# Kernel tuning notes

Hardware: AMD Instinct MI355X
Metric: run time of the kernel (lower is better)

The kernel has to match this reference:

```python
import jax, jax.numpy as jnp
import numpy as np

B, N, P_FEATS = 8, 4096, 3
WIDTH, HEADS, LAYERS, N_LAT = 768, 12, 8, 256
NUM_FREQS = 8
D_HEAD = WIDTH // HEADS
SCALE = 1.0 / np.sqrt(np.sqrt(D_HEAD))  # applied to q and k separately
IN_DIM = 3 * (1 + 2 * NUM_FREQS) + P_FEATS  # 54
EPS = 1e-5


def fourier_embed(pc):
    # pc: [B,N,3] -> [B,N,51] (include_input + sin/cos at freqs 2^0..2^7)
    freqs = (2.0 ** jnp.arange(NUM_FREQS)).astype(pc.dtype)
    ang = pc[..., None] * freqs  # [B,N,3,F]
    ang = ang.reshape(*pc.shape[:-1], 3 * NUM_FREQS)
    return jnp.concatenate([pc, jnp.sin(ang), jnp.cos(ang)], axis=-1)


def layernorm(x, s, b):
    mu = jnp.mean(x, axis=-1, keepdims=True)
    var = jnp.mean(jnp.square(x - mu), axis=-1, keepdims=True)
    return (x - mu) * jax.lax.rsqrt(var + EPS) * s + b


def mh_attn(q, k, v):
    # q: [B,T,H,C], k/v: [B,S,H,C]
    w = jnp.einsum('bthc,bshc->bhts', q * SCALE, k * SCALE)
    w = jax.nn.softmax(w.astype(jnp.float32), axis=-1).astype(q.dtype)
    out = jnp.einsum('bhts,bshc->bthc', w, v)
    return out.reshape(*q.shape[:2], -1)


def setup_inputs() -> dict:
    key = jax.random.key(0)
    ks = iter(jax.random.split(key, 64))
    rn = lambda shape, std=0.02: jax.random.normal(next(ks), shape, jnp.float32) * std
    inp = {
        'pc': jax.random.normal(next(ks), (B, N, 3), jnp.float32),
        'feats': jax.random.uniform(next(ks), (B, N, P_FEATS), jnp.float32),
        'query': rn((N_LAT, WIDTH)),
        'in_W': rn((WIDTH, IN_DIM)), 'in_b': jnp.zeros((WIDTH,)),
        'ca_qkv_W': rn((3 * WIDTH, WIDTH)), 'ca_qkv_b': jnp.zeros((3 * WIDTH,)),
        'ca_proj_W': rn((WIDTH, WIDTH)), 'ca_proj_b': jnp.zeros((WIDTH,)),
        'ln1_s': jnp.ones((LAYERS, WIDTH)), 'ln1_b': jnp.zeros((LAYERS, WIDTH)),
        'qkv_W': rn((LAYERS, 3 * WIDTH, WIDTH)), 'qkv_b': jnp.zeros((LAYERS, 3 * WIDTH)),
        'proj_W': rn((LAYERS, WIDTH, WIDTH)), 'proj_b': jnp.zeros((LAYERS, WIDTH)),
        'ln2_s': jnp.ones((LAYERS, WIDTH)), 'ln2_b': jnp.zeros((LAYERS, WIDTH)),
        'fc_W': rn((LAYERS, 4 * WIDTH, WIDTH)), 'fc_b': jnp.zeros((LAYERS, 4 * WIDTH)),
        'fc2_W': rn((LAYERS, WIDTH, 4 * WIDTH)), 'fc2_b': jnp.zeros((LAYERS, WIDTH)),
    }
    return inp


def _forward(pc, feats, query, in_W, in_b, ca_qkv_W, ca_qkv_b, ca_proj_W, ca_proj_b,
             ln1_s, ln1_b, qkv_W, qkv_b, proj_W, proj_b, ln2_s, ln2_b,
             fc_W, fc_b, fc2_W, fc2_b):
    bs = pc.shape[0]
    data = jnp.concatenate([fourier_embed(pc), feats], axis=-1)  # [B,N,54]
    data = data @ in_W.T + in_b  # [B,N,W]
    q_lat = jnp.broadcast_to(query[None], (bs, N_LAT, WIDTH))

    # --- cross attention (no residual, matching source) ---
    q = (q_lat @ ca_qkv_W.T + ca_qkv_b)[..., :WIDTH]
    kv = data @ ca_qkv_W.T + ca_qkv_b
    k, v = kv[..., WIDTH:2 * WIDTH], kv[..., 2 * WIDTH:]
    q = q.reshape(bs, N_LAT, HEADS, D_HEAD)
    k = k.reshape(bs, N, HEADS, D_HEAD)
    v = v.reshape(bs, N, HEADS, D_HEAD)
    latents = mh_attn(q, k, v) @ ca_proj_W.T + ca_proj_b  # [B,L,W]

    # --- self-attention transformer stack via scan ---
    def block(x, p):
        (l1s, l1b, qW, qb, pW, pb, l2s, l2b, fW, fb, f2W, f2b) = p
        h = layernorm(x, l1s, l1b)
        qkv = (h @ qW.T + qb).reshape(bs, N_LAT, HEADS, 3 * D_HEAD)
        qh, kh, vh = jnp.split(qkv, 3, axis=-1)
        x = x + mh_attn(qh, kh, vh) @ pW.T + pb
        h = layernorm(x, l2s, l2b)
        h = jax.nn.gelu(h @ fW.T + fb, approximate=False) @ f2W.T + f2b
        return x + h, None

    params = (ln1_s, ln1_b, qkv_W, qkv_b, proj_W, proj_b, ln2_s, ln2_b, fc_W, fc_b, fc2_W, fc2_b)
    latents, _ = jax.lax.scan(block, latents, params)
    return latents, pc


def reference(pc, feats, query, in_W, in_b, ca_qkv_W, ca_qkv_b, ca_proj_W, ca_proj_b,
              ln1_s, ln1_b, qkv_W, qkv_b, proj_W, proj_b, ln2_s, ln2_b,
              fc_W, fc_b, fc2_W, fc2_b):
    return _forward(pc, feats, query, in_W, in_b, ca_qkv_W, ca_qkv_b, ca_proj_W, ca_proj_b,
                    ln1_s, ln1_b, qkv_W, qkv_b, proj_W, proj_b, ln2_s, ln2_b,
                    fc_W, fc_b, fc2_W, fc2_b)
```

## Files before the change

### kernel.cpp

```cpp
#include <hip/hip_runtime.h>
#include <stdint.h>

typedef unsigned short u16;
typedef __bf16 bf16x8 __attribute__((ext_vector_type(8)));
typedef float f32x4 __attribute__((ext_vector_type(4)));

#define DEVINL __device__ __forceinline__

DEVINL u16 f2bf(float f) {
  union { float f; unsigned u; } c; c.f = f;
  unsigned u = c.u + 0x7FFFu + ((c.u >> 16) & 1u);
  return (u16)(u >> 16);
}

DEVINL float bf2f(u16 v) {
  union { unsigned u; float f; } c; c.u = (unsigned)v << 16;
  return c.f;
}

DEVINL void gl2lds16(const void* g, void* l) {
  __builtin_amdgcn_global_load_lds(
      (const __attribute__((address_space(1))) unsigned int*)g,
      (__attribute__((address_space(3))) unsigned int*)l, 16, 0, 0);
}

__global__ __launch_bounds__(256) void cvt4_kernel(
    const float* __restrict__ s0, u16* __restrict__ d0, int n0,
    const float* __restrict__ s1, u16* __restrict__ d1, int n1,
    const float* __restrict__ s2, u16* __restrict__ d2, int n2,
    const float* __restrict__ s3, u16* __restrict__ d3, int n3) {
  int i = blockIdx.x * 256 + threadIdx.x;
  const float* s; u16* d;
  if (i < n0) { s = s0; d = d0; }
  else {
    i -= n0;
    if (i < n1) { s = s1; d = d1; }
    else {
      i -= n1;
      if (i < n2) { s = s2; d = d2; }
      else {
        i -= n2;
        if (i >= n3) return;
        s = s3; d = d3;
      }
    }
  }
  float4 v = ((const float4*)s)[i];
  unsigned a = (unsigned)f2bf(v.x) | ((unsigned)f2bf(v.y) << 16);
  unsigned b = (unsigned)f2bf(v.z) | ((unsigned)f2bf(v.w) << 16);
  ((uint2*)d)[i] = make_uint2(a, b);
}

__global__ __launch_bounds__(256) void pad_inw_kernel(const float* __restrict__ src,
                                                      u16* __restrict__ dst) {
  int t = blockIdx.x * 256 + threadIdx.x;
  int r = t >> 6, c = t & 63;
  dst[t] = (c < 54) ? f2bf(src[r * 54 + c]) : (u16)0;
}

__global__ __launch_bounds__(256) void embed_kernel(const float* __restrict__ pc,
                                                    const float* __restrict__ feats,
                                                    u16* __restrict__ emb) {
  int t = blockIdx.x * 256 + threadIdx.x;
  int p = t >> 6, c = t & 63;
  float v = 0.f;
  if (c < 3) {
    v = pc[p * 3 + c];
  } else if (c < 27) {
    int i = c - 3;
    float f = (float)(1 << (i & 7));
    v = sinf(pc[p * 3 + (i >> 3)] * f);
  } else if (c < 51) {
    int i = c - 27;
    float f = (float)(1 << (i & 7));
    v = cosf(pc[p * 3 + (i >> 3)] * f);
  } else if (c < 54) {
    v = feats[p * 3 + (c - 51)];
  }
  emb[t] = f2bf(v);
}

template <int TM, int TN, int WR, int WC, int MODE>
__global__ __launch_bounds__(256) void gemm_t(
    const u16* __restrict__ A, const u16* __restrict__ Bw,
    const float* __restrict__ bias, const float* __restrict__ resid,
    float* __restrict__ outF, u16* __restrict__ outB,
    int M, int N, int Nout, int K, int gelu,
    u16* __restrict__ vt, int vy, int skvt, int bsh) {
  constexpr int IM = TM / WR / 16;
  constexpr int IN = TN / WC / 16;
  __shared__ u16 As[TM * 32];
  __shared__ u16 Bs[TN * 32];
  const int tid = threadIdx.x;
  const int lane = tid & 63, w = tid >> 6;
  const int l15 = lane & 15, quad = lane >> 4;
  const int mblk = blockIdx.x * TM, nblk = blockIdx.y * TN;
  const int wm = (w % WR) * (TM / WR);
  const int wn = (w / WR) * (TN / WC);

  f32x4 acc[IM][IN];
#pragma unroll
  for (int i = 0; i < IM; i++)
#pragma unroll
    for (int j = 0; j < IN; j++) acc[i][j] = f32x4{0.f, 0.f, 0.f, 0.f};

  const bool tv = (MODE == 1) && ((int)blockIdx.y >= vy);

  if (!tv) {
    for (int k0 = 0; k0 < K; k0 += 32) {
#pragma unroll
      for (int s = tid; s < TM * 4; s += 256) {
        int row = s >> 2, c8 = (s & 3) << 3;
        gl2lds16(A + (size_t)(mblk + row) * K + (k0 + c8), &As[s * 8]);
      }
#pragma unroll
      for (int s = tid; s < TN * 4; s += 256) {
        int row = s >> 2, c8 = (s & 3) << 3;
        gl2lds16(Bw + (size_t)(nblk + row) * K + (k0 + c8), &Bs[s * 8]);
      }
      __syncthreads();
      bf16x8 af[IM], bfr[IN];
#pragma unroll
      for (int i = 0; i < IM; i++)
        af[i] = *(const bf16x8*)&As[(wm + i * 16 + l15) * 32 + quad * 8];
#pragma unroll
      for (int j = 0; j < IN; j++)
        bfr[j] = *(const bf16x8*)&Bs[(wn + j * 16 + l15) * 32 + quad * 8];
#pragma unroll
      for (int i = 0; i < IM; i++)
#pragma unroll
        for (int j = 0; j < IN; j++)
          acc[i][j] = __builtin_amdgcn_mfma_f32_16x16x32_bf16(bfr[j], af[i], acc[i][j], 0, 0, 0);
      __syncthreads();
    }
#pragma unroll
    for (int i = 0; i < IM; i++) {
      int m = mblk + wm + i * 16 + l15;
#pragma unroll
      for (int j = 0; j < IN; j++) {
        int n0 = nblk + wn + j * 16 + quad * 4;
        float4 bv = *(const float4*)&bias[n0];
        float v0 = acc[i][j][0] + bv.x;
        float v1 = acc[i][j][1] + bv.y;
        float v2 = acc[i][j][2] + bv.z;
        float v3 = acc[i][j][3] + bv.w;
        if (gelu) {
          v0 = 0.5f * v0 * (1.0f + erff(v0 * 0.70710678118f));
          v1 = 0.5f * v1 * (1.0f + erff(v1 * 0.70710678118f));
          v2 = 0.5f * v2 * (1.0f + erff(v2 * 0.70710678118f));
          v3 = 0.5f * v3 * (1.0f + erff(v3 * 0.70710678118f));
        }
        size_t idx = (size_t)m * Nout + n0;
        if (resid) {
          float4 rv = *(const float4*)&resid[idx];
          v0 += rv.x; v1 += rv.y; v2 += rv.z; v3 += rv.w;
        }
        if (outF) {
          float4 ov = {v0, v1, v2, v3};
          *(float4*)&outF[idx] = ov;
        }
        if (outB) {
          unsigned lo = (unsigned)f2bf(v0) | ((unsigned)f2bf(v1) << 16);
          unsigned hi = (unsigned)f2bf(v2) | ((unsigned)f2bf(v3) << 16);
          *(uint2*)&outB[idx] = make_uint2(lo, hi);
        }
      }
    }
  } else {
    for (int k0 = 0; k0 < K; k0 += 32) {
#pragma unroll
      for (int s = tid; s < TM * 4; s += 256) {
        int row = s >> 2, c8 = (s & 3) << 3;
        gl2lds16(A + (size_t)(mblk + row) * K + (k0 + c8), &As[s * 8]);
      }
#pragma unroll
      for (int s = tid; s < TN * 4; s += 256) {
        int row = s >> 2, c8 = (s & 3) << 3;
        gl2lds16(Bw + (size_t)(nblk + row) * K + (k0 + c8), &Bs[s * 8]);
      }
      __syncthreads();
      bf16x8 af[IM], bfr[IN];
#pragma unroll
      for (int i = 0; i < IM; i++)
        af[i] = *(const bf16x8*)&As[(wm + i * 16 + l15) * 32 + quad * 8];
#pragma unroll
      for (int j = 0; j < IN; j++)
        bfr[j] = *(const bf16x8*)&Bs[(wn + j * 16 + l15) * 32 + quad * 8];
#pragma unroll
      for (int i = 0; i < IM; i++)
#pragma unroll
        for (int j = 0; j < IN; j++)
          acc[i][j] = __builtin_amdgcn_mfma_f32_16x16x32_bf16(af[i], bfr[j], acc[i][j], 0, 0, 0);
      __syncthreads();
    }
    int msk = (1 << bsh) - 1;
#pragma unroll
    for (int j = 0; j < IN; j++) {
      int n = nblk + wn + j * 16 + l15;
      float bv = bias[n];
      int nv = n - vy * TN;
#pragma unroll
      for (int i = 0; i < IM; i++) {
        int m0 = mblk + wm + i * 16 + quad * 4;
        int b = m0 >> bsh;
        int s0 = m0 & msk;
        float v0 = acc[i][j][0] + bv;
        float v1 = acc[i][j][1] + bv;
        float v2 = acc[i][j][2] + bv;
        float v3 = acc[i][j][3] + bv;
        unsigned lo = (unsigned)f2bf(v0) | ((unsigned)f2bf(v1) << 16);
        unsigned hi = (unsigned)f2bf(v2) | ((unsigned)f2bf(v3) << 16);
        size_t addr = (size_t)(b * 768 + nv) * skvt + s0;
        *(uint2*)&vt[addr] = make_uint2(lo, hi);
      }
    }
  }
}

__global__ __launch_bounds__(256) void repack_vt_kernel(
    const u16* __restrict__ In, long bstride, int rs, int voff, int hs,
    u16* __restrict__ Vt, int Skv) {
  __shared__ u16 tile[64 * 65];
  int nst = Skv >> 6;
  int bid = blockIdx.x;
  int st = bid % nst;
  int bh = bid / nst;
  int h = bh % 12, b = bh / 12;
  const u16* src = In + (size_t)b * bstride + (size_t)(st * 64) * rs + voff + h * hs;
  int tid = threadIdx.x;
#pragma unroll
  for (int p = 0; p < 2; p++) {
    int slot = tid + p * 256;
    int s = slot >> 3, d8 = (slot & 7) << 3;
    uint4 v = *(const uint4*)(src + (size_t)s * rs + d8);
    u16 tmp[8];
    *(uint4*)tmp = v;
#pragma unroll
    for (int j = 0; j < 8; j++) tile[s * 65 + d8 + j] = tmp[j];
  }
  __syncthreads();
  u16* dst = Vt + ((size_t)(b * 12 + h) * 64) * Skv + st * 64;
#pragma unroll
  for (int p = 0; p < 2; p++) {
    int slot = tid + p * 256;
    int d = slot >> 3, s8 = (slot & 7) << 3;
    u16 tmp[8];
#pragma unroll
    for (int j = 0; j < 8; j++) tmp[j] = tile[(s8 + j) * 65 + d];
    *(uint4*)(dst + (size_t)d * Skv + s8) = *(uint4*)tmp;
  }
}

__global__ __launch_bounds__(256) void flash_kernel(
    const u16* __restrict__ Q, long qb, int qrs, int qhs,
    const u16* __restrict__ Kp, long kb, int krs, int khs,
    const u16* __restrict__ Vt, u16* __restrict__ Out,
    u16* __restrict__ Part, float* __restrict__ Ml,
    int Skv, int nsplit, int kvlen, float scale2) {
  __shared__ u16 Qs[64 * 64];
  __shared__ u16 Ks[64 * 64];
  __shared__ u16 Vs[64 * 64];
  __shared__ u16 Ps[64 * 72];

  const int tid = threadIdx.x;
  const int lane = tid & 63, w = tid >> 6;
  const int l15 = lane & 15, quad = lane >> 4;

  int bid = blockIdx.x;
  int per_bh = nsplit << 2;
  int bh = bid / per_bh;
  int rem = bid - bh * per_bh;
  int split = rem >> 2, qt = rem & 3;
  int h = bh % 12, b = bh / 12;

  const u16* Qbase = Q + (size_t)b * qb + (size_t)(qt * 64) * qrs + h * qhs;
  const u16* Kbase = Kp + (size_t)b * kb + (size_t)h * khs;
  const u16* Vbase = Vt + ((size_t)(b * 12 + h) * 64) * Skv;

#pragma unroll
  for (int p = 0; p < 2; ++p) {
    int slot = tid + p * 256;
    int row = slot >> 3, c = slot & 7;
    int cg = (c - row) & 7;
    gl2lds16(Qbase + (size_t)row * qrs + cg * 8, &Qs[slot * 8]);
  }
  __syncthreads();

  bf16x8 qa[2];
#pragma unroll
  for (int kk = 0; kk < 2; kk++)
    qa[kk] = *(const bf16x8*)&Qs[(w * 16 + l15) * 64 + ((kk * 4 + quad + l15) & 7) * 8];

  f32x4 zero = {0.f, 0.f, 0.f, 0.f};
  f32x4 O[4];
  float m_i[4], l_i[4];
#pragma unroll
  for (int d = 0; d < 4; d++) O[d] = zero;
#pragma unroll
  for (int r = 0; r < 4; r++) { m_i[r] = -1e30f; l_i[r] = 0.f; }

  int kt0 = split * kvlen;
  for (int kt = kt0; kt < kt0 + kvlen; kt += 64) {
#pragma unroll
    for (int p = 0; p < 2; ++p) {
      int slot = tid + p * 256;
      int row = slot >> 3, c = slot & 7;
      int cg = (c - row) & 7;
      gl2lds16(Kbase + (size_t)(kt + row) * krs + cg * 8, &Ks[slot * 8]);
      gl2lds16(Vbase + (size_t)row * Skv + kt + cg * 8, &Vs[slot * 8]);
    }
    __syncthreads();

    f32x4 S[4];
#pragma unroll
    for (int j = 0; j < 4; j++) S[j] = zero;
#pragma unroll
    for (int kk = 0; kk < 2; kk++) {
#pragma unroll
      for (int j = 0; j < 4; j++) {
        bf16x8 kf = *(const bf16x8*)&Ks[(j * 16 + l15) * 64 + ((kk * 4 + quad + l15) & 7) * 8];
        S[j] = __builtin_amdgcn_mfma_f32_16x16x32_bf16(qa[kk], kf, S[j], 0, 0, 0);
      }
    }
    float alpha[4];
#pragma unroll
    for (int r = 0; r < 4; r++) {
      float s0 = S[0][r] * scale2, s1 = S[1][r] * scale2;
      float s2 = S[2][r] * scale2, s3 = S[3][r] * scale2;
      S[0][r] = s0; S[1][r] = s1; S[2][r] = s2; S[3][r] = s3;
      float mx = fmaxf(fmaxf(s0, s1), fmaxf(s2, s3));
#pragma unroll
      for (int msk = 1; msk < 16; msk <<= 1) mx = fmaxf(mx, __shfl_xor(mx, msk, 64));
      float mnew = fmaxf(m_i[r], mx);
      float al = __expf(m_i[r] - mnew);
      m_i[r] = mnew;
      alpha[r] = al;
      float sum = 0.f;
#pragma unroll
      for (int j = 0; j < 4; j++) {
        float pv = __expf(S[j][r] - mnew);
        S[j][r] = pv;
        sum += pv;
      }
#pragma unroll
      for (int msk = 1; msk < 16; msk <<= 1) sum += __shfl_xor(sum, msk, 64);
      l_i[r] = l_i[r] * al + sum;
    }
#pragma unroll
    for (int j = 0; j < 4; j++)
#pragma unroll
      for (int r = 0; r < 4; r++)
        Ps[(w * 16 + quad * 4 + r) * 72 + j * 16 + l15] = f2bf(S[j][r]);
#pragma unroll
    for (int d = 0; d < 4; d++)
#pragma unroll
      for (int r = 0; r < 4; r++) O[d][r] *= alpha[r];
    __asm__ __volatile__("s_waitcnt lgkmcnt(0)" ::: "memory");
#pragma unroll
    for (int kk = 0; kk < 2; kk++) {
      bf16x8 pa = *(const bf16x8*)&Ps[(w * 16 + l15) * 72 + kk * 32 + quad * 8];
#pragma unroll
      for (int d = 0; d < 4; d++) {
        bf16x8 vf = *(const bf16x8*)&Vs[(d * 16 + l15) * 64 + ((kk * 4 + quad + l15) & 7) * 8];
        O[d] = __builtin_amdgcn_mfma_f32_16x16x32_bf16(pa, vf, O[d], 0, 0, 0);
      }
    }
    __syncthreads();
  }

  if (nsplit == 1) {
    u16* Ob = Out + ((size_t)(b * 256 + qt * 64 + w * 16 + quad * 4)) * 768 + h * 64 + l15;
#pragma unroll
    for (int d = 0; d < 4; d++)
#pragma unroll
      for (int r = 0; r < 4; r++) {
        float v = O[d][r] / l_i[r];
        Ob[(size_t)r * 768 + d * 16] = f2bf(v);
      }
  } else {
    u16* Pb = Part + ((size_t)(bh * 4 + qt) * nsplit + split) * 4096;
    int rowb = w * 16 + quad * 4;
#pragma unroll
    for (int d = 0; d < 4; d++)
#pragma unroll
      for (int r = 0; r < 4; r++)
        Pb[(rowb + r) * 64 + d * 16 + l15] = f2bf(O[d][r]);
    if (l15 == 0) {
      float* MlB = Ml + ((size_t)(bh * 4 + qt) * nsplit + split) * 128;
#pragma unroll
      for (int r = 0; r < 4; r++) {
        MlB[rowb + r] = m_i[r];
        MlB[64 + rowb + r] = l_i[r];
      }
    }
  }
}

__global__ __launch_bounds__(256) void freduce_kernel(
    const u16* __restrict__ Part, const float* __restrict__ Ml,
    u16* __restrict__ Out, int nsplit) {
  int bid = blockIdx.x;
  int qt = bid & 3, bh = bid >> 2;
  int h = bh % 12, b = bh / 12;
  int tid = threadIdx.x;
  int r = tid >> 2, dc = tid & 3;
  const float* mlb = Ml + (size_t)(bh * 4 + qt) * nsplit * 128;
  float M = -1e30f;
  for (int s = 0; s < nsplit; s++) M = fmaxf(M, mlb[s * 128 + r]);
  float L = 0.f;
  float accv[16];
#pragma unroll
  for (int i = 0; i < 16; i++) accv[i] = 0.f;
  const u16* pb = Part + (size_t)(bh * 4 + qt) * nsplit * 4096 + r * 64 + dc * 16;
  for (int s = 0; s < nsplit; s++) {
    float wgt = __expf(mlb[s * 128 + r] - M);
    L += wgt * mlb[s * 128 + 64 + r];
    u16 tmp[16];
    *(uint4*)tmp = *(const uint4*)(pb + s * 4096);
    *(uint4*)(tmp + 8) = *(const uint4*)(pb + s * 4096 + 8);
#pragma unroll
    for (int i = 0; i < 16; i++) accv[i] += wgt * bf2f(tmp[i]);
  }
  float inv = 1.f / L;
  u16 ot[16];
#pragma unroll
  for (int i = 0; i < 16; i++) ot[i] = f2bf(accv[i] * inv);
  u16* ob = Out + ((size_t)(b * 256 + qt * 64 + r)) * 768 + h * 64 + dc * 16;
  *(uint4*)ob = *(uint4*)ot;
  *(uint4*)(ob + 8) = *(uint4*)(ot + 8);
}

__global__ __launch_bounds__(256) void ln_kernel(const float* __restrict__ X,
                                                 const float* __restrict__ sc,
                                                 const float* __restrict__ bi,
                                                 u16* __restrict__ Hout) {
  int row = blockIdx.x;
  int tid = threadIdx.x;
  const float* x = X + (size_t)row * 768;
  float v0 = x[tid], v1 = x[tid + 256], v2 = x[tid + 512];
  float s = v0 + v1 + v2;
  float q = v0 * v0 + v1 * v1 + v2 * v2;
#pragma unroll
  for (int m = 1; m < 64; m <<= 1) {
    s += __shfl_xor(s, m, 64);
    q += __shfl_xor(q, m, 64);
  }
  __shared__ float rs[4], rq[4];
  if ((tid & 63) == 0) { rs[tid >> 6] = s; rq[tid >> 6] = q; }
  __syncthreads();
  s = rs[0] + rs[1] + rs[2] + rs[3];
  q = rq[0] + rq[1] + rq[2] + rq[3];
  float mu = s * (1.f / 768.f);
  float var = q * (1.f / 768.f) - mu * mu;
  float rstd = rsqrtf(var + 1e-5f);
  u16* ho = Hout + (size_t)row * 768;
  ho[tid]       = f2bf((v0 - mu) * rstd * sc[tid]       + bi[tid]);
  ho[tid + 256] = f2bf((v1 - mu) * rstd * sc[tid + 256] + bi[tid + 256]);
  ho[tid + 512] = f2bf((v2 - mu) * rstd * sc[tid + 512] + bi[tid + 512]);
}

__global__ __launch_bounds__(256) void copy4_kernel(const float* __restrict__ src,
                                                    float* __restrict__ dst, int n4) {
  int i = blockIdx.x * 256 + threadIdx.x;
  if (i < n4) ((float4*)dst)[i] = ((const float4*)src)[i];
}

extern "C" void kernel_launch(void* const* d_in, const int* in_sizes, int n_in,
                              void* d_out, int out_size, void* d_ws, size_t ws_size,
                              hipStream_t stream) {
  const float* pc        = (const float*)d_in[0];
  const float* feats     = (const float*)d_in[1];
  const float* query     = (const float*)d_in[2];
  const float* in_W      = (const float*)d_in[3];
  const float* in_b      = (const float*)d_in[4];
  const float* ca_qkv_W  = (const float*)d_in[5];
  const float* ca_qkv_b  = (const float*)d_in[6];
  const float* ca_proj_W = (const float*)d_in[7];
  const float* ca_proj_b = (const float*)d_in[8];
  const float* ln1_s     = (const float*)d_in[9];
  const float* ln1_b     = (const float*)d_in[10];
  const float* qkv_W     = (const float*)d_in[11];
  const float* qkv_b     = (const float*)d_in[12];
  const float* proj_W    = (const float*)d_in[13];
  const float* proj_b    = (const float*)d_in[14];
  const float* ln2_s     = (const float*)d_in[15];
  const float* ln2_b     = (const float*)d_in[16];
  const float* fc_W      = (const float*)d_in[17];
  const float* fc_b      = (const float*)d_in[18];
  const float* fc2_W     = (const float*)d_in[19];
  const float* fc2_b     = (const float*)d_in[20];

  char* base = (char*)d_ws;
  size_t off = 0;
  auto alloc = [&](size_t bytes) -> char* {
    char* p = base + off;
    off += (bytes + 255) & ~(size_t)255;
    return p;
  };

  u16* Wq      = (u16*)alloc(768 * 64 * 2);
  u16* Wquery  = (u16*)alloc(256 * 768 * 2);
  u16* Wcaqkv  = (u16*)alloc(2304 * 768 * 2);
  u16* Wcaproj = (u16*)alloc(768 * 768 * 2);
  u16* Wlqkv   = (u16*)alloc(2304 * 768 * 2);
  u16* Wlproj  = (u16*)alloc(768 * 768 * 2);
  u16* Wlfc    = (u16*)alloc(3072 * 768 * 2);
  u16* Wlfc2   = (u16*)alloc(768 * 3072 * 2);
  u16* qc      = (u16*)alloc(256 * 768 * 2);
  u16* attn    = (u16*)alloc((size_t)2048 * 768 * 2);
  u16* hbuf    = (u16*)alloc((size_t)2048 * 768 * 2);
  char* uni    = alloc(13369344);
  u16* qkvb    = (u16*)uni;
  u16* VtS     = (u16*)(uni + 9437184);
  u16* fc1     = (u16*)uni;
  u16* Part    = (u16*)uni;
  float* Ml    = (float*)(uni + 12582912);

  size_t fixed_end = off;
  size_t per_b = (size_t)4096 * 64 * 2 + 3 * ((size_t)4096 * 768 * 2);
  int CB;
  if (fixed_end + 8 * per_b + 4096 <= ws_size) CB = 8;
  else if (fixed_end + 2 * per_b + 4096 <= ws_size) CB = 2;
  else CB = 1;

  u16* emb   = (u16*)alloc((size_t)CB * 4096 * 64 * 2);
  u16* dataB = (u16*)alloc((size_t)CB * 4096 * 768 * 2);
  u16* kvbK  = (u16*)alloc((size_t)CB * 4096 * 768 * 2);
  u16* VtC   = (u16*)alloc((size_t)CB * 4096 * 768 * 2);

  float* latents = (float*)d_out;
  const float scale2 = 0.125f;

  {
    int n0 = 256 * 768 / 4, n1 = 2304 * 768 / 4, n2 = 768 * 768 / 4;
    cvt4_kernel<<<(n0 + n1 + n2 + 255) / 256, 256, 0, stream>>>(
        query, Wquery, n0, ca_qkv_W, Wcaqkv, n1, ca_proj_W, Wcaproj, n2,
        nullptr, nullptr, 0);
  }
  pad_inw_kernel<<<192, 256, 0, stream>>>(in_W, Wq);

  gemm_t<64, 64, 2, 2, 0><<<dim3(4, 12), 256, 0, stream>>>(
      Wquery, Wcaqkv, ca_qkv_b, nullptr, nullptr, qc,
      256, 768, 768, 768, 0, nullptr, 0, 0, 0);

  int nchunk = 8 / CB;
  for (int c = 0; c < nchunk; ++c) {
    int Mc = CB * 4096;
    const float* pc_c = pc + (size_t)c * Mc * 3;
    const float* ft_c = feats + (size_t)c * Mc * 3;
    embed_kernel<<<Mc / 4, 256, 0, stream>>>(pc_c, ft_c, emb);
    gemm_t<128, 128, 2, 2, 0><<<dim3(Mc / 128, 6), 256, 0, stream>>>(
        emb, Wq, in_b, nullptr, nullptr, dataB,
        Mc, 768, 768, 64, 0, nullptr, 0, 0, 0);
    gemm_t<128, 128, 2, 2, 1><<<dim3(Mc / 128, 12), 256, 0, stream>>>(
        dataB, Wcaqkv + (size_t)768 * 768, ca_qkv_b + 768, nullptr, nullptr, kvbK,
        Mc, 1536, 768, 768, 0, VtC, 6, 4096, 12);
    flash_kernel<<<CB * 12 * 16, 256, 0, stream>>>(
        qc, 0L, 768, 64, kvbK, (long)4096 * 768, 768, 64, VtC,
        nullptr, Part, Ml, 4096, 4, 1024, scale2);
    freduce_kernel<<<CB * 48, 256, 0, stream>>>(
        Part, Ml, attn + (size_t)c * CB * 256 * 768, 4);
  }
  gemm_t<64, 64, 2, 2, 0><<<dim3(32, 12), 256, 0, stream>>>(
      attn, Wcaproj, ca_proj_b, nullptr, latents, nullptr,
      2048, 768, 768, 768, 0, nullptr, 0, 0, 0);

  for (int l = 0; l < 8; ++l) {
    {
      int n0 = 2304 * 768 / 4, n1 = 768 * 768 / 4, n2 = 3072 * 768 / 4, n3 = n2;
      cvt4_kernel<<<(n0 + n1 + n2 + n3 + 255) / 256, 256, 0, stream>>>(
          qkv_W + (size_t)l * 2304 * 768, Wlqkv, n0,
          proj_W + (size_t)l * 768 * 768, Wlproj, n1,
          fc_W + (size_t)l * 3072 * 768, Wlfc, n2,
          fc2_W + (size_t)l * 768 * 3072, Wlfc2, n3);
    }
    ln_kernel<<<2048, 256, 0, stream>>>(latents, ln1_s + l * 768, ln1_b + l * 768, hbuf);
    gemm_t<64, 128, 1, 4, 0><<<dim3(32, 18), 256, 0, stream>>>(
        hbuf, Wlqkv, qkv_b + l * 2304, nullptr, nullptr, qkvb,
        2048, 2304, 2304, 768, 0, nullptr, 0, 0, 0);
    repack_vt_kernel<<<384, 256, 0, stream>>>(qkvb, (long)256 * 2304, 2304, 128, 192, VtS, 256);
    flash_kernel<<<384, 256, 0, stream>>>(
        qkvb, (long)256 * 2304, 2304, 192, qkvb + 64, (long)256 * 2304, 2304, 192,
        VtS, attn, nullptr, nullptr, 256, 1, 256, scale2);
    gemm_t<64, 64, 2, 2, 0><<<dim3(32, 12), 256, 0, stream>>>(
        attn, Wlproj, proj_b + l * 768, latents, latents, nullptr,
        2048, 768, 768, 768, 0, nullptr, 0, 0, 0);
    ln_kernel<<<2048, 256, 0, stream>>>(latents, ln2_s + l * 768, ln2_b + l * 768, hbuf);
    gemm_t<64, 128, 1, 4, 0><<<dim3(32, 24), 256, 0, stream>>>(
        hbuf, Wlfc, fc_b + l * 3072, nullptr, nullptr, fc1,
        2048, 3072, 3072, 768, 1, nullptr, 0, 0, 0);
    gemm_t<64, 64, 2, 2, 0><<<dim3(32, 12), 256, 0, stream>>>(
        fc1, Wlfc2, fc2_b + l * 768, latents, latents, nullptr,
        2048, 768, 768, 3072, 0, nullptr, 0, 0, 0);
  }

  copy4_kernel<<<96, 256, 0, stream>>>(pc, (float*)d_out + (size_t)2048 * 768, 98304 / 4);
}
```

Measured before the change: 1.495 ms.

## Fold input projection into cross-attention KV weights and batch weight conversion

The input linear layer (54->768) and the cross-attention K/V projection (768->1536) are pre-multiplied into a single 64x1536 weight with a combined bias. The per-point GEMM then runs with K=64 instead of materialising the 768-wide data tensor and doing a K=768 GEMM. This removes a large GEMM and an intermediate buffer, at the cost of a small precomputation and extra bf16 rounding of the product weight. Separately, all eight layers' weights are converted to bf16 in one launch when the workspace allows, instead of one conversion per layer.

```diff
diff --git a/kernel.cpp b/kernel.cpp
--- a/kernel.cpp
+++ b/kernel.cpp
@@ -51,11 +51,27 @@
   ((uint2*)d)[i] = make_uint2(a, b);
 }
 
-__global__ __launch_bounds__(256) void pad_inw_kernel(const float* __restrict__ src,
-                                                      u16* __restrict__ dst) {
+__global__ __launch_bounds__(256) void pad_inwT_kernel(const float* __restrict__ src,
+                                                       u16* __restrict__ dst) {
   int t = blockIdx.x * 256 + threadIdx.x;
-  int r = t >> 6, c = t & 63;
-  dst[t] = (c < 54) ? f2bf(src[r * 54 + c]) : (u16)0;
+  if (t >= 64 * 768) return;
+  int j = t / 768, o = t - j * 768;
+  dst[t] = (j < 54) ? f2bf(src[o * 54 + j]) : (u16)0;
+}
+
+__global__ __launch_bounds__(256) void bprime_kernel(const float* __restrict__ caW,
+                                                     const float* __restrict__ caB,
+                                                     const float* __restrict__ inb,
+                                                     float* __restrict__ bp) {
+  int w = threadIdx.x >> 6, lane = threadIdx.x & 63;
+  int m = blockIdx.x * 4 + w;
+  const float* row = caW + (size_t)(768 + m) * 768;
+  float s = 0.f;
+#pragma unroll
+  for (int k = 0; k < 12; k++) s += row[lane + k * 64] * inb[lane + k * 64];
+#pragma unroll
+  for (int msk = 32; msk >= 1; msk >>= 1) s += __shfl_xor(s, msk, 64);
+  if (lane == 0) bp[m] = s + caB[768 + m];
 }
 
 __global__ __launch_bounds__(256) void embed_kernel(const float* __restrict__ pc,
@@ -139,7 +155,7 @@
 #pragma unroll
       for (int j = 0; j < IN; j++) {
         int n0 = nblk + wn + j * 16 + quad * 4;
-        float4 bv = *(const float4*)&bias[n0];
+        float4 bv = bias ? *(const float4*)&bias[n0] : make_float4(0.f, 0.f, 0.f, 0.f);
         float v0 = acc[i][j][0] + bv.x;
         float v1 = acc[i][j][1] + bv.y;
         float v2 = acc[i][j][2] + bv.z;
@@ -197,7 +213,7 @@
 #pragma unroll
     for (int j = 0; j < IN; j++) {
       int n = nblk + wn + j * 16 + l15;
-      float bv = bias[n];
+      float bv = bias ? bias[n] : 0.f;
       int nv = n - vy * TN;
 #pragma unroll
       for (int i = 0; i < IM; i++) {
@@ -498,14 +514,12 @@
     return p;
   };
 
-  u16* Wq      = (u16*)alloc(768 * 64 * 2);
+  u16* WqT     = (u16*)alloc(64 * 768 * 2);
   u16* Wquery  = (u16*)alloc(256 * 768 * 2);
   u16* Wcaqkv  = (u16*)alloc(2304 * 768 * 2);
   u16* Wcaproj = (u16*)alloc(768 * 768 * 2);
-  u16* Wlqkv   = (u16*)alloc(2304 * 768 * 2);
-  u16* Wlproj  = (u16*)alloc(768 * 768 * 2);
-  u16* Wlfc    = (u16*)alloc(3072 * 768 * 2);
-  u16* Wlfc2   = (u16*)alloc(768 * 3072 * 2);
+  u16* Wkp     = (u16*)alloc(1536 * 64 * 2);
+  float* bprime = (float*)alloc(1536 * 4);
   u16* qc      = (u16*)alloc(256 * 768 * 2);
   u16* attn    = (u16*)alloc((size_t)2048 * 768 * 2);
   u16* hbuf    = (u16*)alloc((size_t)2048 * 768 * 2);
@@ -517,16 +531,39 @@
   float* Ml    = (float*)(uni + 12582912);
 
   size_t fixed_end = off;
-  size_t per_b = (size_t)4096 * 64 * 2 + 3 * ((size_t)4096 * 768 * 2);
-  int CB;
-  if (fixed_end + 8 * per_b + 4096 <= ws_size) CB = 8;
-  else if (fixed_end + 2 * per_b + 4096 <= ws_size) CB = 2;
-  else CB = 1;
-
-  u16* emb   = (u16*)alloc((size_t)CB * 4096 * 64 * 2);
-  u16* dataB = (u16*)alloc((size_t)CB * 4096 * 768 * 2);
-  u16* kvbK  = (u16*)alloc((size_t)CB * 4096 * 768 * 2);
-  u16* VtC   = (u16*)alloc((size_t)CB * 4096 * 768 * 2);
+  const size_t wAllSz = (size_t)8 * (2304 * 768 + 768 * 768 + 2 * 3072 * 768) * 2;
+  auto crossSz = [](int cb) {
+    return (size_t)cb * 4096 * 64 * 2 + 2 * ((size_t)cb * 4096 * 768 * 2);
+  };
+
+  bool allw; int CB;
+  if (fixed_end + (wAllSz > crossSz(8) ? wAllSz : crossSz(8)) + 65536 <= ws_size) {
+    allw = true;  CB = 8;
+  } else if (fixed_end + 14155776 + crossSz(2) + 65536 <= ws_size) {
+    allw = false; CB = 2;
+  } else {
+    allw = false; CB = 1;
+  }
+
+  u16 *WqkvB, *WprojB, *WfcB, *Wfc2B, *emb, *kvbK, *VtC;
+  if (allw) {
+    char* X = base + off;
+    WqkvB  = (u16*)X;
+    WprojB = WqkvB + (size_t)8 * 2304 * 768;
+    WfcB   = WprojB + (size_t)8 * 768 * 768;
+    Wfc2B  = WfcB + (size_t)8 * 3072 * 768;
+    emb  = (u16*)X;
+    kvbK = (u16*)(X + (size_t)CB * 4096 * 64 * 2);
+    VtC  = (u16*)(X + (size_t)CB * 4096 * 64 * 2 + (size_t)CB * 4096 * 768 * 2);
+  } else {
+    WqkvB  = (u16*)alloc(2304 * 768 * 2);
+    WprojB = (u16*)alloc(768 * 768 * 2);
+    WfcB   = (u16*)alloc(3072 * 768 * 2);
+    Wfc2B  = (u16*)alloc((size_t)768 * 3072 * 2);
+    emb  = (u16*)alloc((size_t)CB * 4096 * 64 * 2);
+    kvbK = (u16*)alloc((size_t)CB * 4096 * 768 * 2);
+    VtC  = (u16*)alloc((size_t)CB * 4096 * 768 * 2);
+  }
 
   float* latents = (float*)d_out;
   const float scale2 = 0.125f;
@@ -537,7 +574,11 @@
         query, Wquery, n0, ca_qkv_W, Wcaqkv, n1, ca_proj_W, Wcaproj, n2,
         nullptr, nullptr, 0);
   }
-  pad_inw_kernel<<<192, 256, 0, stream>>>(in_W, Wq);
+  pad_inwT_kernel<<<192, 256, 0, stream>>>(in_W, WqT);
+  gemm_t<64, 64, 2, 2, 0><<<dim3(24, 1), 256, 0, stream>>>(
+      Wcaqkv + (size_t)768 * 768, WqT, nullptr, nullptr, nullptr, Wkp,
+      1536, 64, 64, 768, 0, nullptr, 0, 0, 0);
+  bprime_kernel<<<384, 256, 0, stream>>>(ca_qkv_W, ca_qkv_b, in_b, bprime);
 
   gemm_t<64, 64, 2, 2, 0><<<dim3(4, 12), 256, 0, stream>>>(
       Wquery, Wcaqkv, ca_qkv_b, nullptr, nullptr, qc,
@@ -549,12 +590,9 @@
     const float* pc_c = pc + (size_t)c * Mc * 3;
     const float* ft_c = feats + (size_t)c * Mc * 3;
     embed_kernel<<<Mc / 4, 256, 0, stream>>>(pc_c, ft_c, emb);
-    gemm_t<128, 128, 2, 2, 0><<<dim3(Mc / 128, 6), 256, 0, stream>>>(
-        emb, Wq, in_b, nullptr, nullptr, dataB,
-        Mc, 768, 768, 64, 0, nullptr, 0, 0, 0);
     gemm_t<128, 128, 2, 2, 1><<<dim3(Mc / 128, 12), 256, 0, stream>>>(
-        dataB, Wcaqkv + (size_t)768 * 768, ca_qkv_b + 768, nullptr, nullptr, kvbK,
-        Mc, 1536, 768, 768, 0, VtC, 6, 4096, 12);
+        emb, Wkp, bprime, nullptr, nullptr, kvbK,
+        Mc, 1536, 768, 64, 0, VtC, 6, 4096, 12);
     flash_kernel<<<CB * 12 * 16, 256, 0, stream>>>(
         qc, 0L, 768, 64, kvbK, (long)4096 * 768, 768, 64, VtC,
         nullptr, Part, Ml, 4096, 4, 1024, scale2);
@@ -565,32 +603,42 @@
       attn, Wcaproj, ca_proj_b, nullptr, latents, nullptr,
       2048, 768, 768, 768, 0, nullptr, 0, 0, 0);
 
+  if (allw) {
+    int n0 = 8 * 2304 * 768 / 4, n1 = 8 * 768 * 768 / 4, n2 = 8 * 3072 * 768 / 4;
+    cvt4_kernel<<<(n0 + n1 + 2 * n2 + 255) / 256, 256, 0, stream>>>(
+        qkv_W, WqkvB, n0, proj_W, WprojB, n1, fc_W, WfcB, n2, fc2_W, Wfc2B, n2);
+  }
+
   for (int l = 0; l < 8; ++l) {
-    {
-      int n0 = 2304 * 768 / 4, n1 = 768 * 768 / 4, n2 = 3072 * 768 / 4, n3 = n2;
-      cvt4_kernel<<<(n0 + n1 + n2 + n3 + 255) / 256, 256, 0, stream>>>(
-          qkv_W + (size_t)l * 2304 * 768, Wlqkv, n0,
-          proj_W + (size_t)l * 768 * 768, Wlproj, n1,
-          fc_W + (size_t)l * 3072 * 768, Wlfc, n2,
-          fc2_W + (size_t)l * 768 * 3072, Wlfc2, n3);
+    u16* Wlq  = allw ? WqkvB  + (size_t)l * 2304 * 768 : WqkvB;
+    u16* Wlp  = allw ? WprojB + (size_t)l * 768 * 768  : WprojB;
+    u16* Wlf  = allw ? WfcB   + (size_t)l * 3072 * 768 : WfcB;
+    u16* Wlf2 = allw ? Wfc2B  + (size_t)l * 3072 * 768 : Wfc2B;
+    if (!allw) {
+      int n0 = 2304 * 768 / 4, n1 = 768 * 768 / 4, n2 = 3072 * 768 / 4;
+      cvt4_kernel<<<(n0 + n1 + 2 * n2 + 255) / 256, 256, 0, stream>>>(
+          qkv_W + (size_t)l * 2304 * 768, Wlq, n0,
+          proj_W + (size_t)l * 768 * 768, Wlp, n1,
+          fc_W + (size_t)l * 3072 * 768, Wlf, n2,
+          fc2_W + (size_t)l * 768 * 3072, Wlf2, n2);
     }
     ln_kernel<<<2048, 256, 0, stream>>>(latents, ln1_s + l * 768, ln1_b + l * 768, hbuf);
     gemm_t<64, 128, 1, 4, 0><<<dim3(32, 18), 256, 0, stream>>>(
-        hbuf, Wlqkv, qkv_b + l * 2304, nullptr, nullptr, qkvb,
+        hbuf, Wlq, qkv_b + l * 2304, nullptr, nullptr, qkvb,
         2048, 2304, 2304, 768, 0, nullptr, 0, 0, 0);
     repack_vt_kernel<<<384, 256, 0, stream>>>(qkvb, (long)256 * 2304, 2304, 128, 192, VtS, 256);
     flash_kernel<<<384, 256, 0, stream>>>(
         qkvb, (long)256 * 2304, 2304, 192, qkvb + 64, (long)256 * 2304, 2304, 192,
         VtS, attn, nullptr, nullptr, 256, 1, 256, scale2);
     gemm_t<64, 64, 2, 2, 0><<<dim3(32, 12), 256, 0, stream>>>(
-        attn, Wlproj, proj_b + l * 768, latents, latents, nullptr,
+        attn, Wlp, proj_b + l * 768, latents, latents, nullptr,
         2048, 768, 768, 768, 0, nullptr, 0, 0, 0);
     ln_kernel<<<2048, 256, 0, stream>>>(latents, ln2_s + l * 768, ln2_b + l * 768, hbuf);
     gemm_t<64, 128, 1, 4, 0><<<dim3(32, 24), 256, 0, stream>>>(
-        hbuf, Wlfc, fc_b + l * 3072, nullptr, nullptr, fc1,
+        hbuf, Wlf, fc_b + l * 3072, nullptr, nullptr, fc1,
         2048, 3072, 3072, 768, 1, nullptr, 0, 0, 0);
     gemm_t<64, 64, 2, 2, 0><<<dim3(32, 12), 256, 0, stream>>>(
-        fc1, Wlfc2, fc2_b + l * 768, latents, latents, nullptr,
+        fc1, Wlf2, fc2_b + l * 768, latents, latents, nullptr,
         2048, 768, 768, 3072, 0, nullptr, 0, 0, 0);
   }
 
```

After: 1.411 ms. 5.6% less time.
